# Kernel tuning notes

Measured on AMD Instinct MI355X. Metric: run time of the kernel, lower is better.

The kernel has to match this reference:

```python
import jax, jax.numpy as jnp
import numpy as np

N_STACK = 1
SEL_RATE = 0.5


def setup_inputs() -> dict:
    key = jax.random.key(0)
    k1, k2, k3 = jax.random.split(key, 3)
    preds = jax.random.normal(k1, (128, 17, 64, 64), dtype=jnp.float32)
    targets = jax.random.normal(k2, (2, 128, 17, 64, 64), dtype=jnp.float32)
    sampleWeight = jax.random.uniform(k3, (128, 1), dtype=jnp.float32)
    return {"preds": preds, "targets": targets, "sampleWeight": sampleWeight}


def _score_and_thr(v):
    # v: [bs, k, HW]; softmax over joints (dim=-2), max over spatial, global
    # (1 - selRate)-quantile threshold via sort, as in the torch code.
    sm = jax.nn.softmax(v, axis=-2)
    score = jnp.max(sm, axis=-1)                      # [bs, k]
    flat = jnp.sort(score.reshape(-1))
    thr = flat[int(flat.shape[0] * (1.0 - SEL_RATE))]  # scalar
    mask = (score >= thr).astype(v.dtype)             # [bs, k]
    return score, thr, mask


def reference(preds, targets, sampleWeight):
    bs, k = preds.shape[0], preds.shape[1]
    # ensemble mean over models -> pseudo target [bs, k, H, W]
    targets_mean = jnp.mean(targets, axis=0)
    v1 = preds.reshape(bs, k, -1)
    v2 = targets_mean.reshape(bs, k, -1)

    # per-(sample, joint) MSE, weighted
    loss = jnp.mean((v1 - v2) ** 2, axis=-1)          # [bs, k]
    loss = loss * sampleWeight                        # sampleWeight [bs,1] broadcast

    v1_score, thr1, v1_mask = _score_and_thr(v1)
    v2_score, thr2, v2_mask = _score_and_thr(v2)
    mask = v1_mask * v2_mask                          # [bs, k]

    num_pseudo = jnp.sum(loss.reshape(-1) > 0).astype(jnp.int32)
    num_selected = jnp.sum(mask.reshape(-1) > 0).astype(jnp.int32)

    # masked mean over unlabeled samples (sampleWeight > 0) instead of
    # Python-loop filtering: identical math when >=1 positive sample.
    w = (sampleWeight[:, 0] > 0).astype(v1_score.dtype)  # [bs]
    cnt = jnp.sum(w)
    v1_mean = jnp.sum(v1_score * w[:, None], axis=0) / cnt  # [k]
    v2_mean = jnp.sum(v2_score * w[:, None], axis=0) / cnt  # [k]
    joint_score_mean = 0.5 * (v1_mean + v2_mean)             # [k]

    combined_loss = jnp.sum(loss * mask)
    rateThr1 = thr1[None]
    rateThr2 = thr2[None]
    return combined_loss, num_pseudo, num_selected, joint_score_mean, rateThr1, rateThr2
```

## Files before the change

kernel.cpp:

```cpp
#include <hip/hip_runtime.h>

#define BS 128
#define KJ 17
#define HW 4096
#define CHUNKS 16
#define NBLK1 (BS * CHUNKS)
#define NBK (BS * KJ)
#define KSEL 1088

#define PL_OFF 0
#define S1_OFF (NBLK1 * KJ)
#define S2_OFF (2 * NBLK1 * KJ)
#define LW_OFF (3 * NBLK1 * KJ)
#define SA_OFF (LW_OFF + NBK)
#define SB_OFF (SA_OFF + NBK)
#define THR_OFF (SB_OFF + NBK)

typedef float v4f __attribute__((ext_vector_type(4)));

__device__ __forceinline__ float4 ntload4(const float* p) {
    const v4f v = __builtin_nontemporal_load((const v4f*)p);
    return make_float4(v.x, v.y, v.z, v.w);
}

template<int K0, int NK>
__device__ __forceinline__ void team_pass1(const float* __restrict__ pb,
                                           const float* __restrict__ t0b,
                                           const float* __restrict__ t1b,
                                           int ti, float (*lb)[68],
                                           float4* pv, float4* tv,
                                           float4& spP, float4& spT) {
    float4 vb[NK];
#pragma unroll
    for (int j = 0; j < NK; ++j) pv[j] = ntload4(pb + (K0 + j) * HW);
#pragma unroll
    for (int j = 0; j < NK; ++j) tv[j] = ntload4(t0b + (K0 + j) * HW);
#pragma unroll
    for (int j = 0; j < NK; ++j) vb[j] = ntload4(t1b + (K0 + j) * HW);
    spP = make_float4(0.f, 0.f, 0.f, 0.f);
    spT = make_float4(0.f, 0.f, 0.f, 0.f);
#pragma unroll
    for (int j = 0; j < NK; ++j) {
        tv[j].x = 0.5f * (tv[j].x + vb[j].x);
        tv[j].y = 0.5f * (tv[j].y + vb[j].y);
        tv[j].z = 0.5f * (tv[j].z + vb[j].z);
        tv[j].w = 0.5f * (tv[j].w + vb[j].w);
        const float dx = pv[j].x - tv[j].x, dy = pv[j].y - tv[j].y;
        const float dz = pv[j].z - tv[j].z, dw = pv[j].w - tv[j].w;
        lb[K0 + j][ti] = dx * dx + dy * dy + dz * dz + dw * dw;
        spP.x += __expf(pv[j].x); spP.y += __expf(pv[j].y);
        spP.z += __expf(pv[j].z); spP.w += __expf(pv[j].w);
        spT.x += __expf(tv[j].x); spT.y += __expf(tv[j].y);
        spT.z += __expf(tv[j].z); spT.w += __expf(tv[j].w);
    }
}

template<int K0, int NK>
__device__ __forceinline__ void score_write(float (*lb)[68], int ti,
                                            const float4* v, float4 inv) {
#pragma unroll
    for (int j = 0; j < NK; ++j) {
        const float m = fmaxf(fmaxf(__expf(v[j].x) * inv.x, __expf(v[j].y) * inv.y),
                              fmaxf(__expf(v[j].z) * inv.z, __expf(v[j].w) * inv.w));
        lb[K0 + j][ti] = m;
    }
}

__global__ __launch_bounds__(256, 4) void k1_reduce(const float* __restrict__ preds,
                                                    const float* __restrict__ targets,
                                                    float* __restrict__ ws) {
    __shared__ float lb[KJ][68];
    __shared__ float4 sP[4][64];
    __shared__ float4 sT[4][64];
    __shared__ float buf2[KJ][4];

    const int bid = blockIdx.x;
    const int b = bid >> 4;
    const int c = bid & 15;
    const int tid = threadIdx.x;
    const int tm = tid >> 6;
    const int ti = tid & 63;
    const int s0 = (c << 8) | (ti << 2);

    const float* pb  = preds   + (size_t)b * KJ * HW + s0;
    const float* t0b = targets + (size_t)b * KJ * HW + s0;
    const float* t1b = targets + (size_t)(BS + b) * KJ * HW + s0;

    float4 pv[5], tv[5], spP, spT;
    if      (tm == 0) team_pass1<0, 4>(pb, t0b, t1b, ti, lb, pv, tv, spP, spT);
    else if (tm == 1) team_pass1<4, 4>(pb, t0b, t1b, ti, lb, pv, tv, spP, spT);
    else if (tm == 2) team_pass1<8, 4>(pb, t0b, t1b, ti, lb, pv, tv, spP, spT);
    else              team_pass1<12, 5>(pb, t0b, t1b, ti, lb, pv, tv, spP, spT);
    sP[tm][ti] = spP;
    sT[tm][ti] = spT;
    __syncthreads();

    float4 invP, invT;
    {
        const float4 a0 = sP[0][ti], a1 = sP[1][ti], a2 = sP[2][ti], a3 = sP[3][ti];
        invP.x = 1.0f / (a0.x + a1.x + a2.x + a3.x);
        invP.y = 1.0f / (a0.y + a1.y + a2.y + a3.y);
        invP.z = 1.0f / (a0.z + a1.z + a2.z + a3.z);
        invP.w = 1.0f / (a0.w + a1.w + a2.w + a3.w);
        const float4 b0 = sT[0][ti], b1 = sT[1][ti], b2 = sT[2][ti], b3 = sT[3][ti];
        invT.x = 1.0f / (b0.x + b1.x + b2.x + b3.x);
        invT.y = 1.0f / (b0.y + b1.y + b2.y + b3.y);
        invT.z = 1.0f / (b0.z + b1.z + b2.z + b3.z);
        invT.w = 1.0f / (b0.w + b1.w + b2.w + b3.w);
    }

    if (tid < KJ * 4) {
        const int k = tid >> 2, seg = tid & 3;
        float r = 0.f;
#pragma unroll
        for (int i = 0; i < 16; ++i) {
            const int idx = (i + seg * 4) & 15;
            r += lb[k][(seg << 4) + idx];
        }
        buf2[k][seg] = r;
    }
    __syncthreads();

    if (tid < KJ) {
        ws[PL_OFF + bid * KJ + tid] =
            buf2[tid][0] + buf2[tid][1] + buf2[tid][2] + buf2[tid][3];
    }
    if      (tm == 0) score_write<0, 4>(lb, ti, pv, invP);
    else if (tm == 1) score_write<4, 4>(lb, ti, pv, invP);
    else if (tm == 2) score_write<8, 4>(lb, ti, pv, invP);
    else              score_write<12, 5>(lb, ti, pv, invP);
    __syncthreads();

    if (tid < KJ * 4) {
        const int k = tid >> 2, seg = tid & 3;
        float r = 0.f;
#pragma unroll
        for (int i = 0; i < 16; ++i) {
            const int idx = (i + seg * 4) & 15;
            r = fmaxf(r, lb[k][(seg << 4) + idx]);
        }
        buf2[k][seg] = r;
    }
    __syncthreads();

    if (tid < KJ) {
        ws[S1_OFF + bid * KJ + tid] = fmaxf(fmaxf(buf2[tid][0], buf2[tid][1]),
                                            fmaxf(buf2[tid][2], buf2[tid][3]));
    }
    if      (tm == 0) score_write<0, 4>(lb, ti, tv, invT);
    else if (tm == 1) score_write<4, 4>(lb, ti, tv, invT);
    else if (tm == 2) score_write<8, 4>(lb, ti, tv, invT);
    else              score_write<12, 5>(lb, ti, tv, invT);
    __syncthreads();

    if (tid < KJ * 4) {
        const int k = tid >> 2, seg = tid & 3;
        float r = 0.f;
#pragma unroll
        for (int i = 0; i < 16; ++i) {
            const int idx = (i + seg * 4) & 15;
            r = fmaxf(r, lb[k][(seg << 4) + idx]);
        }
        buf2[k][seg] = r;
    }
    __syncthreads();

    if (tid < KJ) {
        ws[S2_OFF + bid * KJ + tid] = fmaxf(fmaxf(buf2[tid][0], buf2[tid][1]),
                                            fmaxf(buf2[tid][2], buf2[tid][3]));
    }
}

__global__ __launch_bounds__(256) void k2_fold(float* __restrict__ ws,
                                               const float* __restrict__ sw) {
    const int e = blockIdx.x * 256 + threadIdx.x;
    if (e >= NBK) return;
    const int b = e / KJ;
    const int k = e - b * KJ;
    float L = 0.f, S1 = 0.f, S2 = 0.f;
#pragma unroll
    for (int c = 0; c < CHUNKS; ++c) {
        const int idx = (b * CHUNKS + c) * KJ + k;
        L += ws[PL_OFF + idx];
        S1 = fmaxf(S1, ws[S1_OFF + idx]);
        S2 = fmaxf(S2, ws[S2_OFF + idx]);
    }
    ws[LW_OFF + e] = L * (1.0f / HW) * sw[b];
    ws[SA_OFF + e] = S1;
    ws[SB_OFF + e] = S2;
}

__global__ __launch_bounds__(256) void k3_select(float* __restrict__ ws) {
    const int w = blockIdx.x * 4 + (threadIdx.x >> 6);
    const int lane = threadIdx.x & 63;
    const int arr = (w >= NBK) ? 1 : 0;
    const int cand = w - arr * NBK;
    const float* sc = ws + (arr ? SB_OFF : SA_OFF);
    const float e = sc[cand];
    int clt = 0, cle = 0;
    for (int j = lane; j < NBK; j += 64) {
        float x = sc[j];
        clt += (x < e) ? 1 : 0;
        cle += (x <= e) ? 1 : 0;
    }
#pragma unroll
    for (int off = 32; off > 0; off >>= 1) {
        clt += __shfl_xor(clt, off, 64);
        cle += __shfl_xor(cle, off, 64);
    }
    if (lane == 0 && clt <= KSEL && KSEL < cle) {
        ws[THR_OFF + arr] = e;
    }
}

__global__ __launch_bounds__(256) void k4_final(const float* __restrict__ ws,
                                                const float* __restrict__ sw,
                                                float* __restrict__ out) {
    const int tid = threadIdx.x;
    const float thrA = ws[THR_OFF + 0];
    const float thrB = ws[THR_OFF + 1];

    float comb = 0.f, np = 0.f, ns = 0.f;
    for (int e = tid; e < NBK; e += 256) {
        const float L  = ws[LW_OFF + e];
        const float s1 = ws[SA_OFF + e];
        const float s2 = ws[SB_OFF + e];
        const float m = (s1 >= thrA && s2 >= thrB) ? 1.f : 0.f;
        comb += L * m;
        np += (L > 0.f) ? 1.f : 0.f;
        ns += m;
    }
#pragma unroll
    for (int off = 32; off > 0; off >>= 1) {
        comb += __shfl_xor(comb, off, 64);
        np   += __shfl_xor(np, off, 64);
        ns   += __shfl_xor(ns, off, 64);
    }
    __shared__ float wr[4][3];
    const int wid = tid >> 6, lane = tid & 63;
    if (lane == 0) { wr[wid][0] = comb; wr[wid][1] = np; wr[wid][2] = ns; }
    __syncthreads();
    if (tid == 0) {
        float C = 0.f, NP = 0.f, NS = 0.f;
#pragma unroll
        for (int i = 0; i < 4; ++i) { C += wr[i][0]; NP += wr[i][1]; NS += wr[i][2]; }
        out[0] = C;
        out[1] = NP;
        out[2] = NS;
        out[20] = thrA;
        out[21] = thrB;
    }
    if (tid < KJ) {
        float a1 = 0.f, a2 = 0.f, cnt = 0.f;
        for (int b = 0; b < BS; ++b) {
            const float wf = (sw[b] > 0.f) ? 1.f : 0.f;
            cnt += wf;
            a1 += ws[SA_OFF + b * KJ + tid] * wf;
            a2 += ws[SB_OFF + b * KJ + tid] * wf;
        }
        out[3 + tid] = 0.5f * (a1 + a2) / cnt;
    }
}

extern "C" void kernel_launch(void* const* d_in, const int* in_sizes, int n_in,
                              void* d_out, int out_size, void* d_ws, size_t ws_size,
                              hipStream_t stream) {
    const float* preds   = (const float*)d_in[0];
    const float* targets = (const float*)d_in[1];
    const float* sw      = (const float*)d_in[2];
    float* out = (float*)d_out;
    float* ws  = (float*)d_ws;

    hipLaunchKernelGGL(k1_reduce, dim3(NBLK1), dim3(256), 0, stream, preds, targets, ws);
    hipLaunchKernelGGL(k2_fold, dim3((NBK + 255) / 256), dim3(256), 0, stream, ws, sw);
    hipLaunchKernelGGL(k3_select, dim3((2 * NBK) / 4), dim3(256), 0, stream, ws);
    hipLaunchKernelGGL(k4_final, dim3(1), dim3(256), 0, stream, ws, sw, out);
}
```

Baseline: 36.34 us.

## Fuse threshold selection into final kernel using shared-memory radix select

```diff
diff --git a/kernel.cpp b/kernel.cpp
--- a/kernel.cpp
+++ b/kernel.cpp
@@ -14,7 +14,6 @@
 #define LW_OFF (3 * NBLK1 * KJ)
 #define SA_OFF (LW_OFF + NBK)
 #define SB_OFF (SA_OFF + NBK)
-#define THR_OFF (SB_OFF + NBK)
 
 typedef float v4f __attribute__((ext_vector_type(4)));
 
@@ -190,42 +189,79 @@
     ws[SB_OFF + e] = S2;
 }
 
-__global__ __launch_bounds__(256) void k3_select(float* __restrict__ ws) {
-    const int w = blockIdx.x * 4 + (threadIdx.x >> 6);
-    const int lane = threadIdx.x & 63;
-    const int arr = (w >= NBK) ? 1 : 0;
-    const int cand = w - arr * NBK;
-    const float* sc = ws + (arr ? SB_OFF : SA_OFF);
-    const float e = sc[cand];
-    int clt = 0, cle = 0;
-    for (int j = lane; j < NBK; j += 64) {
-        float x = sc[j];
-        clt += (x < e) ? 1 : 0;
-        cle += (x <= e) ? 1 : 0;
-    }
-#pragma unroll
-    for (int off = 32; off > 0; off >>= 1) {
-        clt += __shfl_xor(clt, off, 64);
-        cle += __shfl_xor(cle, off, 64);
-    }
-    if (lane == 0 && clt <= KSEL && KSEL < cle) {
-        ws[THR_OFF + arr] = e;
-    }
-}
-
-__global__ __launch_bounds__(256) void k4_final(const float* __restrict__ ws,
-                                                const float* __restrict__ sw,
-                                                float* __restrict__ out) {
-    const int tid = threadIdx.x;
-    const float thrA = ws[THR_OFF + 0];
-    const float thrB = ws[THR_OFF + 1];
+__global__ __launch_bounds__(512) void k34_final(const float* __restrict__ ws,
+                                                 const float* __restrict__ sw,
+                                                 float* __restrict__ out) {
+    __shared__ float sLW[NBK], sSA[NBK], sSB[NBK];
+    __shared__ int hist[4096];
+    __shared__ int wsum[8];
+    __shared__ int sel_bin, sel_rank;
+    __shared__ float thrAB[2];
+    __shared__ float wr[8][3];
+
+    const int t = threadIdx.x;
+    const int lane = t & 63, wid = t >> 6;
+
+    for (int e = t; e < NBK; e += 512) {
+        sLW[e] = ws[LW_OFF + e];
+        sSA[e] = ws[SA_OFF + e];
+        sSB[e] = ws[SB_OFF + e];
+    }
+    __syncthreads();
+
+    for (int arr = 0; arr < 2; ++arr) {
+        const float* sd = arr ? sSB : sSA;
+        unsigned prefix = 0u, mask = 0u;
+        int R = KSEL;
+#pragma unroll
+        for (int lev = 0; lev < 3; ++lev) {
+            const int shift = (lev == 0) ? 19 : (lev == 1) ? 7 : 0;
+            const int nb = (lev == 2) ? 128 : 4096;
+            for (int i = t; i < nb; i += 512) hist[i] = 0;
+            __syncthreads();
+            for (int e = t; e < NBK; e += 512) {
+                const unsigned u = __float_as_uint(sd[e]);
+                if ((u & mask) == prefix)
+                    atomicAdd(&hist[(u >> shift) & (nb - 1)], 1);
+            }
+            __syncthreads();
+            int J, base_bin;
+            if (nb >= 512) { J = nb / 512; base_bin = t * J; }
+            else { J = (t < nb) ? 1 : 0; base_bin = t; }
+            int p = 0;
+            for (int j = 0; j < J; ++j) p += hist[base_bin + j];
+            int inc = p;
+#pragma unroll
+            for (int off = 1; off < 64; off <<= 1) {
+                const int v = __shfl_up(inc, off, 64);
+                if (lane >= off) inc += v;
+            }
+            if (lane == 63) wsum[wid] = inc;
+            __syncthreads();
+            int excl = inc - p;
+            for (int w = 0; w < wid; ++w) excl += wsum[w];
+            int cum = excl;
+            for (int j = 0; j < J; ++j) {
+                const int h = hist[base_bin + j];
+                if (cum <= R && R < cum + h) { sel_bin = base_bin + j; sel_rank = R - cum; }
+                cum += h;
+            }
+            __syncthreads();
+            prefix |= ((unsigned)sel_bin) << shift;
+            mask   |= ((unsigned)(nb - 1)) << shift;
+            R = sel_rank;
+            __syncthreads();
+        }
+        if (t == 0) thrAB[arr] = __uint_as_float(prefix);
+        __syncthreads();
+    }
+
+    const float thrA = thrAB[0], thrB = thrAB[1];
 
     float comb = 0.f, np = 0.f, ns = 0.f;
-    for (int e = tid; e < NBK; e += 256) {
-        const float L  = ws[LW_OFF + e];
-        const float s1 = ws[SA_OFF + e];
-        const float s2 = ws[SB_OFF + e];
-        const float m = (s1 >= thrA && s2 >= thrB) ? 1.f : 0.f;
+    for (int e = t; e < NBK; e += 512) {
+        const float L = sLW[e];
+        const float m = (sSA[e] >= thrA && sSB[e] >= thrB) ? 1.f : 0.f;
         comb += L * m;
         np += (L > 0.f) ? 1.f : 0.f;
         ns += m;
@@ -236,29 +272,37 @@
         np   += __shfl_xor(np, off, 64);
         ns   += __shfl_xor(ns, off, 64);
     }
-    __shared__ float wr[4][3];
-    const int wid = tid >> 6, lane = tid & 63;
     if (lane == 0) { wr[wid][0] = comb; wr[wid][1] = np; wr[wid][2] = ns; }
     __syncthreads();
-    if (tid == 0) {
+    if (t == 0) {
         float C = 0.f, NP = 0.f, NS = 0.f;
 #pragma unroll
-        for (int i = 0; i < 4; ++i) { C += wr[i][0]; NP += wr[i][1]; NS += wr[i][2]; }
+        for (int i = 0; i < 8; ++i) { C += wr[i][0]; NP += wr[i][1]; NS += wr[i][2]; }
         out[0] = C;
         out[1] = NP;
         out[2] = NS;
         out[20] = thrA;
         out[21] = thrB;
     }
-    if (tid < KJ) {
+
+    if (t < KJ * 16) {
+        const int k = t >> 4, l = t & 15;
         float a1 = 0.f, a2 = 0.f, cnt = 0.f;
-        for (int b = 0; b < BS; ++b) {
+#pragma unroll
+        for (int i = 0; i < 8; ++i) {
+            const int b = l + i * 16;
             const float wf = (sw[b] > 0.f) ? 1.f : 0.f;
             cnt += wf;
-            a1 += ws[SA_OFF + b * KJ + tid] * wf;
-            a2 += ws[SB_OFF + b * KJ + tid] * wf;
-        }
-        out[3 + tid] = 0.5f * (a1 + a2) / cnt;
+            a1 += sSA[b * KJ + k] * wf;
+            a2 += sSB[b * KJ + k] * wf;
+        }
+#pragma unroll
+        for (int off = 1; off < 16; off <<= 1) {
+            a1  += __shfl_xor(a1, off, 16);
+            a2  += __shfl_xor(a2, off, 16);
+            cnt += __shfl_xor(cnt, off, 16);
+        }
+        if (l == 0) out[3 + k] = 0.5f * (a1 + a2) / cnt;
     }
 }
 
@@ -273,6 +317,5 @@
 
     hipLaunchKernelGGL(k1_reduce, dim3(NBLK1), dim3(256), 0, stream, preds, targets, ws);
     hipLaunchKernelGGL(k2_fold, dim3((NBK + 255) / 256), dim3(256), 0, stream, ws, sw);
-    hipLaunchKernelGGL(k3_select, dim3((2 * NBK) / 4), dim3(256), 0, stream, ws);
-    hipLaunchKernelGGL(k4_final, dim3(1), dim3(256), 0, stream, ws, sw, out);
-}
+    hipLaunchKernelGGL(k34_final, dim3(1), dim3(512), 0, stream, ws, sw, out);
+}
```

Measured after the change: 38.37 us. +5.6%, slower.
